# Kernel tuning notes

Hardware: AMD Instinct MI355X
Metric: run time of the kernel (lower is better)

The kernel has to match this reference:

```python
import jax, jax.numpy as jnp
import numpy as np

B, H, W, C = 4, 64, 64, 256
DQK = C // 8

def setup_inputs() -> dict:
    key = jax.random.key(0)
    kx, kq, kk, kv = jax.random.split(key, 4)
    x = jax.random.normal(kx, (B, H, W, C), dtype=jnp.float32)
    Wq = jax.random.normal(kq, (C, DQK), dtype=jnp.float32) * 0.05
    Wk = jax.random.normal(kk, (C, DQK), dtype=jnp.float32) * 0.05
    Wv = jax.random.normal(kv, (C, C), dtype=jnp.float32) * 0.05
    gamma = jnp.ones((1,), dtype=jnp.float32)  # nonzero so attention path matters
    return {"x": x, "Wq": Wq, "Wk": Wk, "Wv": Wv, "gamma": gamma}

def reference(x, Wq, Wk, Wv, gamma):
    b, h, w, c = x.shape
    n = h * w
    xf = x.reshape(b, n, c)                      # [B, N, C]
    q = jnp.einsum('bnc,cd->bnd', xf, Wq)        # [B, N, C/8]  (1x1 conv == GEMM)
    k = jnp.einsum('bnc,cd->bnd', xf, Wk)        # [B, N, C/8]
    v = jnp.einsum('bnc,ce->bne', xf, Wv)        # [B, N, C]
    scores = jnp.einsum('bnd,bmd->bnm', q, k)    # [B, N, N], no scaling (as in source)
    attn = jax.nn.softmax(scores, axis=-1)
    out = jnp.einsum('bnm,bme->bne', attn, v)    # [B, N, C]
    out = out.reshape(b, h, w, c)
    return x + gamma * out
```

## Files before the change

### kernel.cpp

```cpp
#include <hip/hip_runtime.h>
#include <stdint.h>

#define BB 4
#define NN 4096
#define CC 256
#define DD 32

typedef __bf16 bf16;
typedef bf16 bf16x4 __attribute__((ext_vector_type(4)));
typedef bf16 bf16x8 __attribute__((ext_vector_type(8)));
typedef float f32x4 __attribute__((ext_vector_type(4)));
typedef unsigned int u32x4 __attribute__((ext_vector_type(4)));

__global__ void prepw_kernel(const float* __restrict__ Wq,
                             const float* __restrict__ Wk,
                             const float* __restrict__ Wv,
                             bf16* __restrict__ WT)
{
    int i = blockIdx.x * 256 + threadIdx.x;
    if (i < 320 * 256) {
        int d = i >> 8, c = i & 255;
        float val;
        if (d < DD)          val = Wq[c * DD + d];
        else if (d < 2 * DD) val = Wk[c * DD + (d - DD)];
        else                 val = Wv[c * CC + (d - 2 * DD)];
        WT[i] = (bf16)val;
    }
}

__global__ __launch_bounds__(256) void proj_kernel(
    const float* __restrict__ x, const bf16* __restrict__ WT,
    bf16* __restrict__ qb, bf16* __restrict__ kb, bf16* __restrict__ vt)
{
    int b = blockIdx.x >> 7, nt = blockIdx.x & 127;
    int n0 = nt << 5;
    int tid = threadIdx.x;
    int w = tid >> 6, lane = tid & 63;
    int lm = lane & 15, g = lane >> 4;
    int rw = w >> 1;
    int ch = w & 1;

    f32x4 acc[10];
    f32x4 zero4 = {0.f, 0.f, 0.f, 0.f};
#pragma unroll
    for (int i = 0; i < 10; ++i) acc[i] = zero4;

    const float* xrow = x + ((size_t)(b * NN) + n0 + rw * 16 + lm) * CC;
    for (int kc = 0; kc < 8; ++kc) {
        f32x4 a0 = *(const f32x4*)(xrow + kc * 32 + g * 8);
        f32x4 a1 = *(const f32x4*)(xrow + kc * 32 + g * 8 + 4);
        bf16x8 a;
        a[0] = (bf16)a0[0]; a[1] = (bf16)a0[1]; a[2] = (bf16)a0[2]; a[3] = (bf16)a0[3];
        a[4] = (bf16)a1[0]; a[5] = (bf16)a1[1]; a[6] = (bf16)a1[2]; a[7] = (bf16)a1[3];
#pragma unroll
        for (int ct = 0; ct < 10; ++ct) {
            int ctg = ch * 10 + ct;
            bf16x8 wv = *(const bf16x8*)(WT + (ctg * 16 + lm) * 256 + kc * 32 + g * 8);
            acc[ct] = __builtin_amdgcn_mfma_f32_16x16x32_bf16(a, wv, acc[ct], 0, 0, 0);
        }
    }

#pragma unroll
    for (int ct = 0; ct < 10; ++ct) {
        int ctg = ch * 10 + ct;
        int col = ctg * 16 + lm;
        if (ctg < 4) {
#pragma unroll
            for (int r = 0; r < 4; ++r) {
                int n = n0 + rw * 16 + g * 4 + r;
                bf16 hv = (bf16)acc[ct][r];
                if (ctg < 2) qb[((size_t)(b * NN) + n) * DD + col] = hv;
                else         kb[((size_t)(b * NN) + n) * DD + (col - DD)] = hv;
            }
        } else {
            int c = col - 64;
            int tile = nt >> 1;
            int nbase = ((nt & 1) * 32 + rw * 16 + g * 4) ^ ((c & 7) << 3);
            bf16x4 pk;
            pk[0] = (bf16)acc[ct][0]; pk[1] = (bf16)acc[ct][1];
            pk[2] = (bf16)acc[ct][2]; pk[3] = (bf16)acc[ct][3];
            size_t off = (((size_t)(b * 64 + tile)) * 256 + c) * 64 + nbase;
            *(bf16x4*)(vt + off) = pk;
        }
    }
}


#define LOADK(KT_, KF) { \
    const bf16* kbase_ = kb + ((size_t)(b * NN) + (size_t)(KT_) * 64) * DD + g * 8; \
    KF[0] = *(const bf16x8*)(kbase_ + (lm +  0) * DD); \
    KF[1] = *(const bf16x8*)(kbase_ + (lm + 16) * DD); \
    KF[2] = *(const bf16x8*)(kbase_ + (lm + 32) * DD); \
    KF[3] = *(const bf16x8*)(kbase_ + (lm + 48) * DD); }

#define LOADV(KT_, VB) { \
    const bf16* vtile_ = vt + ((size_t)(b * 64 + (KT_))) * 16384; \
    _Pragma("unroll") \
    for (int ct_ = 0; ct_ < 4; ++ct_) { \
        int c_ = 64 * w + 16 * ct_ + lm; \
        const bf16* vrow_ = vtile_ + c_ * 64; \
        int vsw_ = (c_ & 7) << 3; \
        VB[ct_][0] = *(const bf16x8*)(vrow_ + ((8 * g) ^ vsw_)); \
        VB[ct_][1] = *(const bf16x8*)(vrow_ + ((32 + 8 * g) ^ vsw_)); \
    } }

#define PVBLOCK(PRV_, VB) { \
    const float* alph_p = (const float*)(lds + 16384 + (PRV_) * 512); \
    const uint32_t* flg_p = (const uint32_t*)(lds + 16384 + (PRV_) * 512 + 256); \
    const unsigned char* Pp_ = lds + (PRV_) * 8192; \
    u32x4 fl_ = *(const u32x4*)flg_p; \
    if ((fl_[0] & fl_[1] & fl_[2] & fl_[3]) == 0u) { \
        _Pragma("unroll") for (int rt_ = 0; rt_ < 4; ++rt_) { \
            f32x4 a_ = *(const f32x4*)(alph_p + rt_ * 16 + 4 * g); \
            _Pragma("unroll") for (int ct_ = 0; ct_ < 4; ++ct_) { \
                acc[rt_][ct_][0] *= a_[0]; acc[rt_][ct_][1] *= a_[1]; \
                acc[rt_][ct_][2] *= a_[2]; acc[rt_][ct_][3] *= a_[3]; \
            } \
        } \
    } \
    int psw_ = (lm & 7) << 4; \
    _Pragma("unroll") for (int rt_ = 0; rt_ < 4; ++rt_) { \
        const unsigned char* pr_ = Pp_ + (rt_ * 16 + lm) * 128; \
        bf16x8 pa0_ = *(const bf16x8*)(pr_ + (( 0 + 16 * g) ^ psw_)); \
        bf16x8 pa1_ = *(const bf16x8*)(pr_ + ((64 + 16 * g) ^ psw_)); \
        _Pragma("unroll") for (int ct_ = 0; ct_ < 4; ++ct_) { \
            acc[rt_][ct_] = __builtin_amdgcn_mfma_f32_16x16x32_bf16(pa0_, VB[ct_][0], acc[rt_][ct_], 0, 0, 0); \
            acc[rt_][ct_] = __builtin_amdgcn_mfma_f32_16x16x32_bf16(pa1_, VB[ct_][1], acc[rt_][ct_], 0, 0, 0); \
        } \
    } \
}

#define STEP(T_, KF, KFN, VBP, DOPV) { \
    const int cur_ = (T_) & 1; \
    __builtin_amdgcn_s_setprio(1); \
    f32x4 sv0 = __builtin_amdgcn_mfma_f32_16x16x32_bf16(KF[0], qf, zero4, 0, 0, 0); \
    f32x4 sv1 = __builtin_amdgcn_mfma_f32_16x16x32_bf16(KF[1], qf, zero4, 0, 0, 0); \
    f32x4 sv2 = __builtin_amdgcn_mfma_f32_16x16x32_bf16(KF[2], qf, zero4, 0, 0, 0); \
    f32x4 sv3 = __builtin_amdgcn_mfma_f32_16x16x32_bf16(KF[3], qf, zero4, 0, 0, 0); \
    int ktn_ = ((T_) + 1 < kt1) ? ((T_) + 1) : (kt1 - 1); \
    LOADK(ktn_, KFN); \
    if (DOPV) { PVBLOCK(cur_ ^ 1, VBP); } \
    __builtin_amdgcn_s_setprio(0); \
    LOADV(ktn_, VBP); \
    float mx_ = fmaxf(fmaxf(fmaxf(sv0[0], sv0[1]), fmaxf(sv0[2], sv0[3])), \
                      fmaxf(fmaxf(sv1[0], sv1[1]), fmaxf(sv1[2], sv1[3]))); \
    mx_ = fmaxf(mx_, fmaxf(fmaxf(sv2[0], sv2[1]), fmaxf(sv2[2], sv2[3]))); \
    mx_ = fmaxf(mx_, fmaxf(fmaxf(sv3[0], sv3[1]), fmaxf(sv3[2], sv3[3]))); \
    mx_ = fmaxf(mx_, __shfl_xor(mx_, 16)); \
    mx_ = fmaxf(mx_, __shfl_xor(mx_, 32)); \
    float alpha_; \
    int wave_ok_ = __all(mx_ <= mrun + 8.0f); \
    if (!wave_ok_) { float mn_ = fmaxf(mrun, mx_); alpha_ = __expf(mrun - mn_); mrun = mn_; } \
    else alpha_ = 1.0f; \
    float ssum_; \
    { \
        _Pragma("unroll") for (int j_ = 0; j_ < 4; ++j_) sv0[j_] = __expf(sv0[j_] - mrun); \
        _Pragma("unroll") for (int j_ = 0; j_ < 4; ++j_) sv1[j_] = __expf(sv1[j_] - mrun); \
        _Pragma("unroll") for (int j_ = 0; j_ < 4; ++j_) sv2[j_] = __expf(sv2[j_] - mrun); \
        _Pragma("unroll") for (int j_ = 0; j_ < 4; ++j_) sv3[j_] = __expf(sv3[j_] - mrun); \
        f32x4 t_ = (sv0 + sv1) + (sv2 + sv3); \
        ssum_ = (t_[0] + t_[1]) + (t_[2] + t_[3]); \
        ssum_ += __shfl_xor(ssum_, 16); \
        ssum_ += __shfl_xor(ssum_, 32); \
    } \
    lrun = lrun * alpha_ + ssum_; \
    unsigned char* Pb_ = lds + cur_ * 8192; \
    { \
        int rb_ = (16 * w + lm) * 128; \
        int sw_ = (lm & 7) << 4; \
        bf16x4 pk_; \
        pk_[0] = (bf16)sv0[0]; pk_[1] = (bf16)sv0[1]; pk_[2] = (bf16)sv0[2]; pk_[3] = (bf16)sv0[3]; \
        *(bf16x4*)(Pb_ + rb_ + (( 0 + 8 * g) ^ sw_)) = pk_; \
        pk_[0] = (bf16)sv1[0]; pk_[1] = (bf16)sv1[1]; pk_[2] = (bf16)sv1[2]; pk_[3] = (bf16)sv1[3]; \
        *(bf16x4*)(Pb_ + rb_ + ((32 + 8 * g) ^ sw_)) = pk_; \
        pk_[0] = (bf16)sv2[0]; pk_[1] = (bf16)sv2[1]; pk_[2] = (bf16)sv2[2]; pk_[3] = (bf16)sv2[3]; \
        *(bf16x4*)(Pb_ + rb_ + ((64 + 8 * g) ^ sw_)) = pk_; \
        pk_[0] = (bf16)sv3[0]; pk_[1] = (bf16)sv3[1]; pk_[2] = (bf16)sv3[2]; pk_[3] = (bf16)sv3[3]; \
        *(bf16x4*)(Pb_ + rb_ + ((96 + 8 * g) ^ sw_)) = pk_; \
    } \
    float* alph_ = (float*)(lds + 16384 + cur_ * 512); \
    uint32_t* flg_ = (uint32_t*)(lds + 16384 + cur_ * 512 + 256); \
    if (g == 0) alph_[16 * w + lm] = alpha_; \
    if (lane == 0) flg_[w] = (uint32_t)wave_ok_; \
    asm volatile("s_waitcnt lgkmcnt(0)" ::: "memory"); \
    __builtin_amdgcn_s_barrier(); \
    asm volatile("" ::: "memory"); \
}

__global__ __launch_bounds__(256, 2) void attn_kernel(
    const bf16* __restrict__ qb, const bf16* __restrict__ kb,
    const bf16* __restrict__ vt, const float* __restrict__ x,
    const float* __restrict__ gamma, bf16* __restrict__ pacc,
    float* __restrict__ pml, float* __restrict__ out, int KS)
{
    __shared__ __align__(16) unsigned char lds[17408];
    int bid = blockIdx.x;
    int b, qt, ks;
    if (KS == 2) {
        int xcd = bid & 7, slot = bid >> 3;
        b = xcd >> 1;
        int idx = (xcd & 1) * 64 + slot;
        qt = idx >> 1; ks = idx & 1;
    } else {
        ks = bid % KS; int t = bid / KS; b = t >> 6; qt = t & 63;
    }
    int bq = b * 64 + qt;
    int n0 = qt << 6;
    int tid = threadIdx.x;
    int w = tid >> 6, lane = tid & 63;
    int lm = lane & 15, g = lane >> 4;

    bf16x8 qf = *(const bf16x8*)(qb + ((size_t)(b * NN) + n0 + w * 16 + lm) * DD + g * 8);

    f32x4 acc[4][4];
    f32x4 zero4 = {0.f, 0.f, 0.f, 0.f};
#pragma unroll
    for (int i = 0; i < 4; ++i)
#pragma unroll
        for (int j = 0; j < 4; ++j) acc[i][j] = zero4;
    float mrun = -1e30f, lrun = 0.f;

    int KT = 64 / KS;
    int kt0 = ks * KT;
    int kt1 = kt0 + KT;

    bf16x8 kfA[4], kfB[4];
    bf16x8 vbA[4][2], vbB[4][2];
    LOADK(kt0, kfA);
    LOADV(kt0, vbA);

    STEP(kt0, kfA, kfB, vbB, 0);

    int kt = kt0 + 1;
    while (kt + 2 <= kt1) {
        STEP(kt,     kfB, kfA, vbA, 1);
        STEP(kt + 1, kfA, kfB, vbB, 1);
        kt += 2;
    }
    if (kt < kt1) {
        STEP(kt, kfB, kfA, vbA, 1);
    }
    PVBLOCK(1, vbB);

    if (KS == 1) {
        __syncthreads();
        float* lsh = (float*)(lds + 16384);
        if (g == 0) lsh[16 * w + lm] = lrun;
        __syncthreads();
        float gam = gamma[0];
#pragma unroll
        for (int rt = 0; rt < 4; ++rt) {
            f32x4 lv = *(const f32x4*)(lsh + rt * 16 + 4 * g);
            f32x4 inv;
            inv[0] = 1.f / lv[0]; inv[1] = 1.f / lv[1];
            inv[2] = 1.f / lv[2]; inv[3] = 1.f / lv[3];
#pragma unroll
            for (int ct = 0; ct < 4; ++ct) {
                int col = 64 * w + 16 * ct + lm;
#pragma unroll
                for (int r = 0; r < 4; ++r) {
                    int n = n0 + rt * 16 + 4 * g + r;
                    size_t idx = ((size_t)(b * NN) + n) * CC + col;
                    out[idx] = x[idx] + gam * acc[rt][ct][r] * inv[r];
                }
            }
        }
    } else {
        bf16* pa = pacc + ((size_t)(bq * KS + ks)) * (64 * 256);
#pragma unroll
        for (int rt = 0; rt < 4; ++rt) {
#pragma unroll
            for (int ct = 0; ct < 4; ++ct) {
                int col = 64 * w + 16 * ct + lm;
#pragma unroll
                for (int r = 0; r < 4; ++r) {
                    int rowin = rt * 16 + 4 * g + r;
                    pa[rowin * 256 + col] = (bf16)acc[rt][ct][r];
                }
            }
        }
        if (g == 0) {
            int rowin = 16 * w + lm;
            size_t mo = ((size_t)(bq * KS + ks) * 64 + rowin) * 2;
            pml[mo + 0] = mrun;
            pml[mo + 1] = lrun;
        }
    }
}

__global__ __launch_bounds__(256) void combine_kernel(
    const bf16* __restrict__ pacc, const float* __restrict__ pml,
    const float* __restrict__ x, const float* __restrict__ gamma,
    float* __restrict__ out, int KS)
{
    int tid = threadIdx.x;
    int row = blockIdx.x * 4 + (tid >> 6);
    int lane = tid & 63;
    int bq = row >> 6;
    int r64 = row & 63;

    float m[4], l[4];
    float M = -3e38f;
    for (int ks = 0; ks < KS; ++ks) {
        size_t mo = ((size_t)(bq * KS + ks) * 64 + r64) * 2;
        m[ks] = pml[mo + 0];
        l[ks] = pml[mo + 1];
        M = fmaxf(M, m[ks]);
    }
    float L = 0.f;
    float wgt[4];
    for (int ks = 0; ks < KS; ++ks) {
        wgt[ks] = __expf(m[ks] - M);
        L += wgt[ks] * l[ks];
    }
    float s = gamma[0] / L;

    f32x4 a = {0.f, 0.f, 0.f, 0.f};
    for (int ks = 0; ks < KS; ++ks) {
        const bf16* pa = pacc + ((size_t)(bq * KS + ks) * 64 + r64) * 256;
        bf16x4 v = *(const bf16x4*)(pa + lane * 4);
        a[0] += wgt[ks] * (float)v[0]; a[1] += wgt[ks] * (float)v[1];
        a[2] += wgt[ks] * (float)v[2]; a[3] += wgt[ks] * (float)v[3];
    }
    const f32x4* xv = (const f32x4*)(x + (size_t)row * 256);
    f32x4 xi = xv[lane];
    f32x4 o;
    o[0] = xi[0] + s * a[0]; o[1] = xi[1] + s * a[1];
    o[2] = xi[2] + s * a[2]; o[3] = xi[3] + s * a[3];
    ((f32x4*)(out + (size_t)row * 256))[lane] = o;
}

extern "C" void kernel_launch(void* const* d_in, const int* in_sizes, int n_in,
                              void* d_out, int out_size, void* d_ws, size_t ws_size,
                              hipStream_t stream)
{
    const float* x     = (const float*)d_in[0];
    const float* Wq    = (const float*)d_in[1];
    const float* Wk    = (const float*)d_in[2];
    const float* Wv    = (const float*)d_in[3];
    const float* gamma = (const float*)d_in[4];
    float* out = (float*)d_out;

    char* ws = (char*)d_ws;
    bf16* WT = (bf16*)(ws);
    bf16* qb = (bf16*)(ws + 163840);
    bf16* kb = (bf16*)(ws + 1212416);
    bf16* vt = (bf16*)(ws + 2260992);

    const size_t base = 10649600;
    size_t need2 = base + (size_t)2 * (8388608 + 131072);
    int KS = (ws_size >= need2) ? 2 : 1;

    bf16*  pacc = (bf16*)(ws + base);
    float* pml  = (float*)(ws + base + (size_t)KS * 8388608);

    hipLaunchKernelGGL(prepw_kernel, dim3(320), dim3(256), 0, stream,
                       Wq, Wk, Wv, WT);
    hipLaunchKernelGGL(proj_kernel, dim3(512), dim3(256), 0, stream,
                       x, WT, qb, kb, vt);
    hipLaunchKernelGGL(attn_kernel, dim3(256 * KS), dim3(256), 0, stream,
                       qb, kb, vt, x, gamma, pacc, pml, out, KS);
    if (KS > 1) {
        hipLaunchKernelGGL(combine_kernel, dim3(BB * NN / 4), dim3(256), 0, stream,
                           pacc, pml, x, gamma, out, KS);
    }
}
```

Measured before the change: 91.86 us.

## Warp-specialize attention into QK/softmax and PV waves, drop split-K combine

The attention kernel now runs 512 threads per block. Even waves compute QK scores and the softmax and write P to LDS, while odd waves load V and do the PV MFMAs, with the two groups synchronised by barriers. The split-K path and the combine kernel are removed, so each block covers all 64 key tiles for its query tile, giving 256 blocks. The log2(e) factor is folded into Wq so exp2 replaces expf, and the rescale threshold is scaled to match. This aims to overlap softmax work with matrix work and avoid the partial-result round trip, but it loses the extra parallelism from split-K and leaves roughly one block per CU.

```diff
diff --git a/kernel.cpp b/kernel.cpp
--- a/kernel.cpp
+++ b/kernel.cpp
@@ -21,7 +21,7 @@
     if (i < 320 * 256) {
         int d = i >> 8, c = i & 255;
         float val;
-        if (d < DD)          val = Wq[c * DD + d];
+        if (d < DD)          val = Wq[c * DD + d] * 1.4426950408889634f;
         else if (d < 2 * DD) val = Wk[c * DD + (d - DD)];
         else                 val = Wv[c * CC + (d - 2 * DD)];
         WT[i] = (bf16)val;
@@ -97,7 +97,7 @@
     const bf16* vtile_ = vt + ((size_t)(b * 64 + (KT_))) * 16384; \
     _Pragma("unroll") \
     for (int ct_ = 0; ct_ < 4; ++ct_) { \
-        int c_ = 64 * w + 16 * ct_ + lm; \
+        int c_ = 64 * sub + 16 * ct_ + lm; \
         const bf16* vrow_ = vtile_ + c_ * 64; \
         int vsw_ = (c_ & 7) << 3; \
         VB[ct_][0] = *(const bf16x8*)(vrow_ + ((8 * g) ^ vsw_)); \
@@ -119,6 +119,7 @@
         } \
     } \
     int psw_ = (lm & 7) << 4; \
+    __builtin_amdgcn_s_setprio(1); \
     _Pragma("unroll") for (int rt_ = 0; rt_ < 4; ++rt_) { \
         const unsigned char* pr_ = Pp_ + (rt_ * 16 + lm) * 128; \
         bf16x8 pa0_ = *(const bf16x8*)(pr_ + (( 0 + 16 * g) ^ psw_)); \
@@ -128,20 +129,22 @@
             acc[rt_][ct_] = __builtin_amdgcn_mfma_f32_16x16x32_bf16(pa1_, VB[ct_][1], acc[rt_][ct_], 0, 0, 0); \
         } \
     } \
-}
-
-#define STEP(T_, KF, KFN, VBP, DOPV) { \
+    __builtin_amdgcn_s_setprio(0); \
+}
+
+#define PVSTEP(T_, VB) { \
+    PVBLOCK((((T_) - 1) & 1), VB); \
+    int ktn_ = ((T_) + 1 < 64) ? (T_) + 1 : 63; \
+    LOADV(ktn_, VB); }
+
+#define QKSTEP(T_, KF, KFN) { \
     const int cur_ = (T_) & 1; \
-    __builtin_amdgcn_s_setprio(1); \
     f32x4 sv0 = __builtin_amdgcn_mfma_f32_16x16x32_bf16(KF[0], qf, zero4, 0, 0, 0); \
     f32x4 sv1 = __builtin_amdgcn_mfma_f32_16x16x32_bf16(KF[1], qf, zero4, 0, 0, 0); \
     f32x4 sv2 = __builtin_amdgcn_mfma_f32_16x16x32_bf16(KF[2], qf, zero4, 0, 0, 0); \
     f32x4 sv3 = __builtin_amdgcn_mfma_f32_16x16x32_bf16(KF[3], qf, zero4, 0, 0, 0); \
-    int ktn_ = ((T_) + 1 < kt1) ? ((T_) + 1) : (kt1 - 1); \
+    int ktn_ = ((T_) + 1 < 64) ? (T_) + 1 : 63; \
     LOADK(ktn_, KFN); \
-    if (DOPV) { PVBLOCK(cur_ ^ 1, VBP); } \
-    __builtin_amdgcn_s_setprio(0); \
-    LOADV(ktn_, VBP); \
     float mx_ = fmaxf(fmaxf(fmaxf(sv0[0], sv0[1]), fmaxf(sv0[2], sv0[3])), \
                       fmaxf(fmaxf(sv1[0], sv1[1]), fmaxf(sv1[2], sv1[3]))); \
     mx_ = fmaxf(mx_, fmaxf(fmaxf(sv2[0], sv2[1]), fmaxf(sv2[2], sv2[3]))); \
@@ -149,15 +152,15 @@
     mx_ = fmaxf(mx_, __shfl_xor(mx_, 16)); \
     mx_ = fmaxf(mx_, __shfl_xor(mx_, 32)); \
     float alpha_; \
-    int wave_ok_ = __all(mx_ <= mrun + 8.0f); \
-    if (!wave_ok_) { float mn_ = fmaxf(mrun, mx_); alpha_ = __expf(mrun - mn_); mrun = mn_; } \
+    int wave_ok_ = __all(mx_ <= mrun + 11.5f); \
+    if (!wave_ok_) { float mn_ = fmaxf(mrun, mx_); alpha_ = __builtin_exp2f(mrun - mn_); mrun = mn_; } \
     else alpha_ = 1.0f; \
     float ssum_; \
     { \
-        _Pragma("unroll") for (int j_ = 0; j_ < 4; ++j_) sv0[j_] = __expf(sv0[j_] - mrun); \
-        _Pragma("unroll") for (int j_ = 0; j_ < 4; ++j_) sv1[j_] = __expf(sv1[j_] - mrun); \
-        _Pragma("unroll") for (int j_ = 0; j_ < 4; ++j_) sv2[j_] = __expf(sv2[j_] - mrun); \
-        _Pragma("unroll") for (int j_ = 0; j_ < 4; ++j_) sv3[j_] = __expf(sv3[j_] - mrun); \
+        _Pragma("unroll") for (int j_ = 0; j_ < 4; ++j_) sv0[j_] = __builtin_exp2f(sv0[j_] - mrun); \
+        _Pragma("unroll") for (int j_ = 0; j_ < 4; ++j_) sv1[j_] = __builtin_exp2f(sv1[j_] - mrun); \
+        _Pragma("unroll") for (int j_ = 0; j_ < 4; ++j_) sv2[j_] = __builtin_exp2f(sv2[j_] - mrun); \
+        _Pragma("unroll") for (int j_ = 0; j_ < 4; ++j_) sv3[j_] = __builtin_exp2f(sv3[j_] - mrun); \
         f32x4 t_ = (sv0 + sv1) + (sv2 + sv3); \
         ssum_ = (t_[0] + t_[1]) + (t_[2] + t_[3]); \
         ssum_ += __shfl_xor(ssum_, 16); \
@@ -166,7 +169,7 @@
     lrun = lrun * alpha_ + ssum_; \
     unsigned char* Pb_ = lds + cur_ * 8192; \
     { \
-        int rb_ = (16 * w + lm) * 128; \
+        int rb_ = (16 * sub + lm) * 128; \
         int sw_ = (lm & 7) << 4; \
         bf16x4 pk_; \
         pk_[0] = (bf16)sv0[0]; pk_[1] = (bf16)sv0[1]; pk_[2] = (bf16)sv0[2]; pk_[3] = (bf16)sv0[3]; \
@@ -180,73 +183,75 @@
     } \
     float* alph_ = (float*)(lds + 16384 + cur_ * 512); \
     uint32_t* flg_ = (uint32_t*)(lds + 16384 + cur_ * 512 + 256); \
-    if (g == 0) alph_[16 * w + lm] = alpha_; \
-    if (lane == 0) flg_[w] = (uint32_t)wave_ok_; \
+    if (g == 0) alph_[16 * sub + lm] = alpha_; \
+    if (lane == 0) flg_[sub] = (uint32_t)wave_ok_; \
     asm volatile("s_waitcnt lgkmcnt(0)" ::: "memory"); \
-    __builtin_amdgcn_s_barrier(); \
-    asm volatile("" ::: "memory"); \
-}
-
-__global__ __launch_bounds__(256, 2) void attn_kernel(
+}
+
+__global__ __launch_bounds__(512, 2) void attn_kernel(
     const bf16* __restrict__ qb, const bf16* __restrict__ kb,
     const bf16* __restrict__ vt, const float* __restrict__ x,
-    const float* __restrict__ gamma, bf16* __restrict__ pacc,
-    float* __restrict__ pml, float* __restrict__ out, int KS)
+    const float* __restrict__ gamma, float* __restrict__ out)
 {
     __shared__ __align__(16) unsigned char lds[17408];
     int bid = blockIdx.x;
-    int b, qt, ks;
-    if (KS == 2) {
-        int xcd = bid & 7, slot = bid >> 3;
-        b = xcd >> 1;
-        int idx = (xcd & 1) * 64 + slot;
-        qt = idx >> 1; ks = idx & 1;
-    } else {
-        ks = bid % KS; int t = bid / KS; b = t >> 6; qt = t & 63;
-    }
-    int bq = b * 64 + qt;
+    int xcd = bid & 7, slot = bid >> 3;
+    int b = xcd >> 1;
+    int qt = (xcd & 1) * 32 + slot;
     int n0 = qt << 6;
     int tid = threadIdx.x;
     int w = tid >> 6, lane = tid & 63;
     int lm = lane & 15, g = lane >> 4;
-
-    bf16x8 qf = *(const bf16x8*)(qb + ((size_t)(b * NN) + n0 + w * 16 + lm) * DD + g * 8);
-
+    int qk = (w & 1) == 0;
+    int sub = w >> 1;
+
+    f32x4 zero4 = {0.f, 0.f, 0.f, 0.f};
     f32x4 acc[4][4];
-    f32x4 zero4 = {0.f, 0.f, 0.f, 0.f};
 #pragma unroll
     for (int i = 0; i < 4; ++i)
 #pragma unroll
         for (int j = 0; j < 4; ++j) acc[i][j] = zero4;
     float mrun = -1e30f, lrun = 0.f;
 
-    int KT = 64 / KS;
-    int kt0 = ks * KT;
-    int kt1 = kt0 + KT;
-
+    bf16x8 qf{};
     bf16x8 kfA[4], kfB[4];
     bf16x8 vbA[4][2], vbB[4][2];
-    LOADK(kt0, kfA);
-    LOADV(kt0, vbA);
-
-    STEP(kt0, kfA, kfB, vbB, 0);
-
-    int kt = kt0 + 1;
-    while (kt + 2 <= kt1) {
-        STEP(kt,     kfB, kfA, vbA, 1);
-        STEP(kt + 1, kfA, kfB, vbB, 1);
+
+    if (qk) {
+        qf = *(const bf16x8*)(qb + ((size_t)(b * NN) + n0 + sub * 16 + lm) * DD + g * 8);
+        LOADK(0, kfA);
+    } else {
+        LOADV(0, vbA);
+    }
+
+    if (qk) { QKSTEP(0, kfA, kfB); }
+    else    { LOADV(1, vbB); }
+    __builtin_amdgcn_s_barrier();
+    asm volatile("" ::: "memory");
+
+    int kt = 1;
+    while (kt <= 61) {
+        if (qk) { QKSTEP(kt, kfB, kfA); } else { PVSTEP(kt, vbA); }
+        __builtin_amdgcn_s_barrier();
+        asm volatile("" ::: "memory");
+        if (qk) { QKSTEP(kt + 1, kfA, kfB); } else { PVSTEP(kt + 1, vbB); }
+        __builtin_amdgcn_s_barrier();
+        asm volatile("" ::: "memory");
         kt += 2;
     }
-    if (kt < kt1) {
-        STEP(kt, kfB, kfA, vbA, 1);
-    }
-    PVBLOCK(1, vbB);
-
-    if (KS == 1) {
-        __syncthreads();
-        float* lsh = (float*)(lds + 16384);
-        if (g == 0) lsh[16 * w + lm] = lrun;
-        __syncthreads();
+    if (qk) { QKSTEP(63, kfB, kfA); } else { PVSTEP(63, vbA); }
+    __builtin_amdgcn_s_barrier();
+    asm volatile("" ::: "memory");
+
+    float* lsh = (float*)(lds + 16384);
+    if (qk && g == 0) lsh[16 * sub + lm] = lrun;
+    asm volatile("s_waitcnt lgkmcnt(0)" ::: "memory");
+    __builtin_amdgcn_s_barrier();
+    asm volatile("" ::: "memory");
+
+    if (!qk) {
+        PVBLOCK(1, vbB);
+
         float gam = gamma[0];
 #pragma unroll
         for (int rt = 0; rt < 4; ++rt) {
@@ -256,7 +261,7 @@
             inv[2] = 1.f / lv[2]; inv[3] = 1.f / lv[3];
 #pragma unroll
             for (int ct = 0; ct < 4; ++ct) {
-                int col = 64 * w + 16 * ct + lm;
+                int col = 64 * sub + 16 * ct + lm;
 #pragma unroll
                 for (int r = 0; r < 4; ++r) {
                     int n = n0 + rt * 16 + 4 * g + r;
@@ -265,69 +270,7 @@
                 }
             }
         }
-    } else {
-        bf16* pa = pacc + ((size_t)(bq * KS + ks)) * (64 * 256);
-#pragma unroll
-        for (int rt = 0; rt < 4; ++rt) {
-#pragma unroll
-            for (int ct = 0; ct < 4; ++ct) {
-                int col = 64 * w + 16 * ct + lm;
-#pragma unroll
-                for (int r = 0; r < 4; ++r) {
-                    int rowin = rt * 16 + 4 * g + r;
-                    pa[rowin * 256 + col] = (bf16)acc[rt][ct][r];
-                }
-            }
-        }
-        if (g == 0) {
-            int rowin = 16 * w + lm;
-            size_t mo = ((size_t)(bq * KS + ks) * 64 + rowin) * 2;
-            pml[mo + 0] = mrun;
-            pml[mo + 1] = lrun;
-        }
-    }
-}
-
-__global__ __launch_bounds__(256) void combine_kernel(
-    const bf16* __restrict__ pacc, const float* __restrict__ pml,
-    const float* __restrict__ x, const float* __restrict__ gamma,
-    float* __restrict__ out, int KS)
-{
-    int tid = threadIdx.x;
-    int row = blockIdx.x * 4 + (tid >> 6);
-    int lane = tid & 63;
-    int bq = row >> 6;
-    int r64 = row & 63;
-
-    float m[4], l[4];
-    float M = -3e38f;
-    for (int ks = 0; ks < KS; ++ks) {
-        size_t mo = ((size_t)(bq * KS + ks) * 64 + r64) * 2;
-        m[ks] = pml[mo + 0];
-        l[ks] = pml[mo + 1];
-        M = fmaxf(M, m[ks]);
-    }
-    float L = 0.f;
-    float wgt[4];
-    for (int ks = 0; ks < KS; ++ks) {
-        wgt[ks] = __expf(m[ks] - M);
-        L += wgt[ks] * l[ks];
-    }
-    float s = gamma[0] / L;
-
-    f32x4 a = {0.f, 0.f, 0.f, 0.f};
-    for (int ks = 0; ks < KS; ++ks) {
-        const bf16* pa = pacc + ((size_t)(bq * KS + ks) * 64 + r64) * 256;
-        bf16x4 v = *(const bf16x4*)(pa + lane * 4);
-        a[0] += wgt[ks] * (float)v[0]; a[1] += wgt[ks] * (float)v[1];
-        a[2] += wgt[ks] * (float)v[2]; a[3] += wgt[ks] * (float)v[3];
-    }
-    const f32x4* xv = (const f32x4*)(x + (size_t)row * 256);
-    f32x4 xi = xv[lane];
-    f32x4 o;
-    o[0] = xi[0] + s * a[0]; o[1] = xi[1] + s * a[1];
-    o[2] = xi[2] + s * a[2]; o[3] = xi[3] + s * a[3];
-    ((f32x4*)(out + (size_t)row * 256))[lane] = o;
+    }
 }
 
 extern "C" void kernel_launch(void* const* d_in, const int* in_sizes, int n_in,
@@ -347,21 +290,10 @@
     bf16* kb = (bf16*)(ws + 1212416);
     bf16* vt = (bf16*)(ws + 2260992);
 
-    const size_t base = 10649600;
-    size_t need2 = base + (size_t)2 * (8388608 + 131072);
-    int KS = (ws_size >= need2) ? 2 : 1;
-
-    bf16*  pacc = (bf16*)(ws + base);
-    float* pml  = (float*)(ws + base + (size_t)KS * 8388608);
-
     hipLaunchKernelGGL(prepw_kernel, dim3(320), dim3(256), 0, stream,
                        Wq, Wk, Wv, WT);
     hipLaunchKernelGGL(proj_kernel, dim3(512), dim3(256), 0, stream,
                        x, WT, qb, kb, vt);
-    hipLaunchKernelGGL(attn_kernel, dim3(256 * KS), dim3(256), 0, stream,
-                       qb, kb, vt, x, gamma, pacc, pml, out, KS);
-    if (KS > 1) {
-        hipLaunchKernelGGL(combine_kernel, dim3(BB * NN / 4), dim3(256), 0, stream,
-                           pacc, pml, x, gamma, out, KS);
-    }
-}
+    hipLaunchKernelGGL(attn_kernel, dim3(256), dim3(512), 0, stream,
+                       qb, kb, vt, x, gamma, out);
+}
```

New measurement: 98.51 us. 1.07x slower.

## Switch PV product to 32x32x16 MFMA and fold log2e into Wq for exp2

Applied to the files above, without the earlier changes.

Reorganizes the P·V accumulation from 16x16x32 MFMA tiles to 32x32x16 tiles, changing the V fragment layout, the P LDS read pattern, the rescale and the epilogue indexing. This halves the number of MFMA issues and the A/B fragment loads per tile. It also pre-scales Wq by log2(e) so softmax can use exp2 directly, and widens the lazy-rescale threshold to match the base-2 scale. Setprio is moved to wrap only the PV block. The risks are extra register pressure from the larger accumulators and getting the 32x32 output-lane mapping right.

```diff
diff --git a/kernel.cpp b/kernel.cpp
--- a/kernel.cpp
+++ b/kernel.cpp
@@ -10,6 +10,7 @@
 typedef bf16 bf16x4 __attribute__((ext_vector_type(4)));
 typedef bf16 bf16x8 __attribute__((ext_vector_type(8)));
 typedef float f32x4 __attribute__((ext_vector_type(4)));
+typedef float f32x16 __attribute__((ext_vector_type(16)));
 typedef unsigned int u32x4 __attribute__((ext_vector_type(4)));
 
 __global__ void prepw_kernel(const float* __restrict__ Wq,
@@ -21,7 +22,7 @@
     if (i < 320 * 256) {
         int d = i >> 8, c = i & 255;
         float val;
-        if (d < DD)          val = Wq[c * DD + d];
+        if (d < DD)          val = Wq[c * DD + d] * 1.4426950408889634f;
         else if (d < 2 * DD) val = Wk[c * DD + (d - DD)];
         else                 val = Wv[c * CC + (d - 2 * DD)];
         WT[i] = (bf16)val;
@@ -96,12 +97,14 @@
 #define LOADV(KT_, VB) { \
     const bf16* vtile_ = vt + ((size_t)(b * 64 + (KT_))) * 16384; \
     _Pragma("unroll") \
-    for (int ct_ = 0; ct_ < 4; ++ct_) { \
-        int c_ = 64 * w + 16 * ct_ + lm; \
+    for (int ct2_ = 0; ct2_ < 2; ++ct2_) { \
+        int c_ = 64 * w + 32 * ct2_ + l31; \
         const bf16* vrow_ = vtile_ + c_ * 64; \
         int vsw_ = (c_ & 7) << 3; \
-        VB[ct_][0] = *(const bf16x8*)(vrow_ + ((8 * g) ^ vsw_)); \
-        VB[ct_][1] = *(const bf16x8*)(vrow_ + ((32 + 8 * g) ^ vsw_)); \
+        _Pragma("unroll") \
+        for (int ks_ = 0; ks_ < 4; ++ks_) { \
+            VB[ct2_][ks_] = *(const bf16x8*)(vrow_ + ((16 * ks_ + 8 * h) ^ vsw_)); \
+        } \
     } }
 
 #define PVBLOCK(PRV_, VB) { \
@@ -110,29 +113,33 @@
     const unsigned char* Pp_ = lds + (PRV_) * 8192; \
     u32x4 fl_ = *(const u32x4*)flg_p; \
     if ((fl_[0] & fl_[1] & fl_[2] & fl_[3]) == 0u) { \
-        _Pragma("unroll") for (int rt_ = 0; rt_ < 4; ++rt_) { \
-            f32x4 a_ = *(const f32x4*)(alph_p + rt_ * 16 + 4 * g); \
-            _Pragma("unroll") for (int ct_ = 0; ct_ < 4; ++ct_) { \
-                acc[rt_][ct_][0] *= a_[0]; acc[rt_][ct_][1] *= a_[1]; \
-                acc[rt_][ct_][2] *= a_[2]; acc[rt_][ct_][3] *= a_[3]; \
+        _Pragma("unroll") for (int qt2_ = 0; qt2_ < 2; ++qt2_) { \
+            _Pragma("unroll") for (int r2_ = 0; r2_ < 4; ++r2_) { \
+                f32x4 a_ = *(const f32x4*)(alph_p + 32 * qt2_ + 8 * r2_ + 4 * h); \
+                _Pragma("unroll") for (int ct2_ = 0; ct2_ < 2; ++ct2_) { \
+                    _Pragma("unroll") for (int j_ = 0; j_ < 4; ++j_) \
+                        acc32[qt2_][ct2_][4 * r2_ + j_] *= a_[j_]; \
+                } \
             } \
         } \
     } \
-    int psw_ = (lm & 7) << 4; \
-    _Pragma("unroll") for (int rt_ = 0; rt_ < 4; ++rt_) { \
-        const unsigned char* pr_ = Pp_ + (rt_ * 16 + lm) * 128; \
-        bf16x8 pa0_ = *(const bf16x8*)(pr_ + (( 0 + 16 * g) ^ psw_)); \
-        bf16x8 pa1_ = *(const bf16x8*)(pr_ + ((64 + 16 * g) ^ psw_)); \
-        _Pragma("unroll") for (int ct_ = 0; ct_ < 4; ++ct_) { \
-            acc[rt_][ct_] = __builtin_amdgcn_mfma_f32_16x16x32_bf16(pa0_, VB[ct_][0], acc[rt_][ct_], 0, 0, 0); \
-            acc[rt_][ct_] = __builtin_amdgcn_mfma_f32_16x16x32_bf16(pa1_, VB[ct_][1], acc[rt_][ct_], 0, 0, 0); \
+    __builtin_amdgcn_s_setprio(1); \
+    _Pragma("unroll") for (int qt2_ = 0; qt2_ < 2; ++qt2_) { \
+        const unsigned char* pr_ = Pp_ + (32 * qt2_ + l31) * 128; \
+        int psw_ = (l31 & 7) << 4; \
+        _Pragma("unroll") for (int ks_ = 0; ks_ < 4; ++ks_) { \
+            bf16x8 pa_ = *(const bf16x8*)(pr_ + ((32 * ks_ + 16 * h) ^ psw_)); \
+            _Pragma("unroll") for (int ct2_ = 0; ct2_ < 2; ++ct2_) { \
+                acc32[qt2_][ct2_] = __builtin_amdgcn_mfma_f32_32x32x16_bf16( \
+                    pa_, VB[ct2_][ks_], acc32[qt2_][ct2_], 0, 0, 0); \
+            } \
         } \
     } \
+    __builtin_amdgcn_s_setprio(0); \
 }
 
 #define STEP(T_, KF, KFN, VBP, DOPV) { \
     const int cur_ = (T_) & 1; \
-    __builtin_amdgcn_s_setprio(1); \
     f32x4 sv0 = __builtin_amdgcn_mfma_f32_16x16x32_bf16(KF[0], qf, zero4, 0, 0, 0); \
     f32x4 sv1 = __builtin_amdgcn_mfma_f32_16x16x32_bf16(KF[1], qf, zero4, 0, 0, 0); \
     f32x4 sv2 = __builtin_amdgcn_mfma_f32_16x16x32_bf16(KF[2], qf, zero4, 0, 0, 0); \
@@ -140,7 +147,6 @@
     int ktn_ = ((T_) + 1 < kt1) ? ((T_) + 1) : (kt1 - 1); \
     LOADK(ktn_, KFN); \
     if (DOPV) { PVBLOCK(cur_ ^ 1, VBP); } \
-    __builtin_amdgcn_s_setprio(0); \
     LOADV(ktn_, VBP); \
     float mx_ = fmaxf(fmaxf(fmaxf(sv0[0], sv0[1]), fmaxf(sv0[2], sv0[3])), \
                       fmaxf(fmaxf(sv1[0], sv1[1]), fmaxf(sv1[2], sv1[3]))); \
@@ -149,15 +155,15 @@
     mx_ = fmaxf(mx_, __shfl_xor(mx_, 16)); \
     mx_ = fmaxf(mx_, __shfl_xor(mx_, 32)); \
     float alpha_; \
-    int wave_ok_ = __all(mx_ <= mrun + 8.0f); \
-    if (!wave_ok_) { float mn_ = fmaxf(mrun, mx_); alpha_ = __expf(mrun - mn_); mrun = mn_; } \
+    int wave_ok_ = __all(mx_ <= mrun + 11.5f); \
+    if (!wave_ok_) { float mn_ = fmaxf(mrun, mx_); alpha_ = __builtin_exp2f(mrun - mn_); mrun = mn_; } \
     else alpha_ = 1.0f; \
     float ssum_; \
     { \
-        _Pragma("unroll") for (int j_ = 0; j_ < 4; ++j_) sv0[j_] = __expf(sv0[j_] - mrun); \
-        _Pragma("unroll") for (int j_ = 0; j_ < 4; ++j_) sv1[j_] = __expf(sv1[j_] - mrun); \
-        _Pragma("unroll") for (int j_ = 0; j_ < 4; ++j_) sv2[j_] = __expf(sv2[j_] - mrun); \
-        _Pragma("unroll") for (int j_ = 0; j_ < 4; ++j_) sv3[j_] = __expf(sv3[j_] - mrun); \
+        _Pragma("unroll") for (int j_ = 0; j_ < 4; ++j_) sv0[j_] = __builtin_exp2f(sv0[j_] - mrun); \
+        _Pragma("unroll") for (int j_ = 0; j_ < 4; ++j_) sv1[j_] = __builtin_exp2f(sv1[j_] - mrun); \
+        _Pragma("unroll") for (int j_ = 0; j_ < 4; ++j_) sv2[j_] = __builtin_exp2f(sv2[j_] - mrun); \
+        _Pragma("unroll") for (int j_ = 0; j_ < 4; ++j_) sv3[j_] = __builtin_exp2f(sv3[j_] - mrun); \
         f32x4 t_ = (sv0 + sv1) + (sv2 + sv3); \
         ssum_ = (t_[0] + t_[1]) + (t_[2] + t_[3]); \
         ssum_ += __shfl_xor(ssum_, 16); \
@@ -209,15 +215,18 @@
     int tid = threadIdx.x;
     int w = tid >> 6, lane = tid & 63;
     int lm = lane & 15, g = lane >> 4;
+    int l31 = lane & 31, h = lane >> 5;
 
     bf16x8 qf = *(const bf16x8*)(qb + ((size_t)(b * NN) + n0 + w * 16 + lm) * DD + g * 8);
 
-    f32x4 acc[4][4];
+    f32x16 acc32[2][2];
+#pragma unroll
+    for (int i = 0; i < 2; ++i)
+#pragma unroll
+        for (int j = 0; j < 2; ++j)
+#pragma unroll
+            for (int r = 0; r < 16; ++r) acc32[i][j][r] = 0.f;
     f32x4 zero4 = {0.f, 0.f, 0.f, 0.f};
-#pragma unroll
-    for (int i = 0; i < 4; ++i)
-#pragma unroll
-        for (int j = 0; j < 4; ++j) acc[i][j] = zero4;
     float mrun = -1e30f, lrun = 0.f;
 
     int KT = 64 / KS;
@@ -225,22 +234,22 @@
     int kt1 = kt0 + KT;
 
     bf16x8 kfA[4], kfB[4];
-    bf16x8 vbA[4][2], vbB[4][2];
+    bf16x8 vA[2][4], vB[2][4];
     LOADK(kt0, kfA);
-    LOADV(kt0, vbA);
-
-    STEP(kt0, kfA, kfB, vbB, 0);
+    LOADV(kt0, vA);
+
+    STEP(kt0, kfA, kfB, vB, 0);
 
     int kt = kt0 + 1;
     while (kt + 2 <= kt1) {
-        STEP(kt,     kfB, kfA, vbA, 1);
-        STEP(kt + 1, kfA, kfB, vbB, 1);
+        STEP(kt,     kfB, kfA, vA, 1);
+        STEP(kt + 1, kfA, kfB, vB, 1);
         kt += 2;
     }
     if (kt < kt1) {
-        STEP(kt, kfB, kfA, vbA, 1);
-    }
-    PVBLOCK(1, vbB);
+        STEP(kt, kfB, kfA, vA, 1);
+    }
+    PVBLOCK(1, vB);
 
     if (KS == 1) {
         __syncthreads();
@@ -249,33 +258,36 @@
         __syncthreads();
         float gam = gamma[0];
 #pragma unroll
-        for (int rt = 0; rt < 4; ++rt) {
-            f32x4 lv = *(const f32x4*)(lsh + rt * 16 + 4 * g);
-            f32x4 inv;
-            inv[0] = 1.f / lv[0]; inv[1] = 1.f / lv[1];
-            inv[2] = 1.f / lv[2]; inv[3] = 1.f / lv[3];
-#pragma unroll
-            for (int ct = 0; ct < 4; ++ct) {
-                int col = 64 * w + 16 * ct + lm;
-#pragma unroll
-                for (int r = 0; r < 4; ++r) {
-                    int n = n0 + rt * 16 + 4 * g + r;
-                    size_t idx = ((size_t)(b * NN) + n) * CC + col;
-                    out[idx] = x[idx] + gam * acc[rt][ct][r] * inv[r];
+        for (int qt2 = 0; qt2 < 2; ++qt2) {
+#pragma unroll
+            for (int r2 = 0; r2 < 4; ++r2) {
+                f32x4 lv = *(const f32x4*)(lsh + 32 * qt2 + 8 * r2 + 4 * h);
+                f32x4 inv;
+                inv[0] = 1.f / lv[0]; inv[1] = 1.f / lv[1];
+                inv[2] = 1.f / lv[2]; inv[3] = 1.f / lv[3];
+#pragma unroll
+                for (int ct2 = 0; ct2 < 2; ++ct2) {
+                    int col = 64 * w + 32 * ct2 + l31;
+#pragma unroll
+                    for (int j = 0; j < 4; ++j) {
+                        int n = n0 + 32 * qt2 + 8 * r2 + 4 * h + j;
+                        size_t idx = ((size_t)(b * NN) + n) * CC + col;
+                        out[idx] = x[idx] + gam * acc32[qt2][ct2][4 * r2 + j] * inv[j];
+                    }
                 }
             }
         }
     } else {
         bf16* pa = pacc + ((size_t)(bq * KS + ks)) * (64 * 256);
 #pragma unroll
-        for (int rt = 0; rt < 4; ++rt) {
-#pragma unroll
-            for (int ct = 0; ct < 4; ++ct) {
-                int col = 64 * w + 16 * ct + lm;
-#pragma unroll
-                for (int r = 0; r < 4; ++r) {
-                    int rowin = rt * 16 + 4 * g + r;
-                    pa[rowin * 256 + col] = (bf16)acc[rt][ct][r];
+        for (int qt2 = 0; qt2 < 2; ++qt2) {
+#pragma unroll
+            for (int ct2 = 0; ct2 < 2; ++ct2) {
+                int col = 64 * w + 32 * ct2 + l31;
+#pragma unroll
+                for (int reg = 0; reg < 16; ++reg) {
+                    int rowin = 32 * qt2 + (reg & 3) + 8 * (reg >> 2) + 4 * h;
+                    pa[rowin * 256 + col] = (bf16)acc32[qt2][ct2][reg];
                 }
             }
         }
@@ -310,7 +322,7 @@
     float L = 0.f;
     float wgt[4];
     for (int ks = 0; ks < KS; ++ks) {
-        wgt[ks] = __expf(m[ks] - M);
+        wgt[ks] = __builtin_exp2f(m[ks] - M);
         L += wgt[ks] * l[ks];
     }
     float s = gamma[0] / L;
```

After: 99.16 us. 1.08x slower.
